# Kernel optimization log

Measured on AMD Instinct MI355X. Metric: run time of the kernel, lower is better.

The kernel has to match this reference:

```python
import jax, jax.numpy as jnp
import numpy as np

D_MODEL = 1024
NHEAD = 16
HEAD_DIM = D_MODEL // NHEAD
SCALE = HEAD_DIM ** (-0.5)


def setup_inputs() -> dict:
    key = jax.random.key(0)
    k1, k2, k3 = jax.random.split(key, 3)
    B, T, C = 2, 2048, D_MODEL
    x = jax.random.normal(k1, (B, T, C), dtype=jnp.float32)
    W_qkv = jax.random.normal(k2, (3 * C, C), dtype=jnp.float32) * (C ** -0.5)
    b_qkv = jnp.zeros((3 * C,), dtype=jnp.float32)
    W_out = jax.random.normal(k3, (C, C), dtype=jnp.float32) * (C ** -0.5)
    b_out = jnp.zeros((C,), dtype=jnp.float32)
    return {"x": x, "W_qkv": W_qkv, "b_qkv": b_qkv, "W_out": W_out, "b_out": b_out}


def reference(x, W_qkv, b_qkv, W_out, b_out):
    B, T, C = x.shape
    H, hd = NHEAD, HEAD_DIM
    qkv = x @ W_qkv.T + b_qkv
    qkv = qkv.reshape(B, T, 3, H, hd).transpose(2, 0, 3, 1, 4)
    q, k, v = qkv[0], qkv[1], qkv[2]
    # scaled dot-product scores: (B,H,T,T)
    attn = jnp.einsum('bhqd,bhkd->bhqk', q, k) * SCALE
    # causal mask (is_causal=True): lower-triangular allowed
    causal = jnp.tril(jnp.ones((T, T), dtype=bool))
    attn = jnp.where(causal[None, None, :, :], attn, -jnp.inf)
    attn = jax.nn.softmax(attn, axis=-1)
    # (B,H,T,hd) -> (B,T,C)
    out = jnp.einsum('bhqk,bhkd->bhqd', attn, v)
    out = out.transpose(0, 2, 1, 3).reshape(B, T, C)
    out = out @ W_out.T + b_out
    return out
```

## Files before the change

### kernel.cpp

```cpp
#include <hip/hip_runtime.h>
#include <hip/hip_bf16.h>
#include <stdint.h>

#define D_MODEL 1024
#define NHEAD   16
#define HEAD_DIM 64
#define BATCH   2
#define SEQ     2048
#define M_TOK   (BATCH*SEQ)
#define N_QKV   (3*D_MODEL)
#define KDIM    1024
#define Q_SCALE (0.125f * 1.44269504088896f)

typedef __bf16 bf16_t;
typedef bf16_t bf16x8 __attribute__((ext_vector_type(8)));
typedef bf16_t bf16x4 __attribute__((ext_vector_type(4)));
typedef float  f32x4  __attribute__((ext_vector_type(4)));

__device__ __forceinline__ void gl_lds16(const void* g, void* l) {
    __builtin_amdgcn_global_load_lds(
        (__attribute__((address_space(1))) void*)(void*)(const_cast<void*>(g)),
        (__attribute__((address_space(3))) void*)l, 16, 0, 0);
}

#define N4_X  (M_TOK * KDIM / 4)
#define N4_W1 (N_QKV * KDIM / 4)
#define N4_W2 (D_MODEL * KDIM / 4)
__global__ void convert_all(const float* __restrict__ x,
                            const float* __restrict__ w1,
                            const float* __restrict__ w2,
                            bf16_t* __restrict__ ox,
                            bf16_t* __restrict__ o1,
                            bf16_t* __restrict__ o2) {
    int t = blockIdx.x * blockDim.x + threadIdx.x;
    const float* src;
    bf16_t* dst;
    int off;
    if (t < N4_X)                { src = x;  dst = ox; off = t; }
    else if (t < N4_X + N4_W1)   { src = w1; dst = o1; off = t - N4_X; }
    else                         { src = w2; dst = o2; off = t - N4_X - N4_W1; }
    float4 v = reinterpret_cast<const float4*>(src)[off];
    bf16x4 o = { (bf16_t)v.x, (bf16_t)v.y, (bf16_t)v.z, (bf16_t)v.w };
    reinterpret_cast<bf16x4*>(dst)[off] = o;
}

template <int MODE>
__global__ __launch_bounds__(256) void gemm_bt(
    const bf16_t* __restrict__ A,
    const bf16_t* __restrict__ Bw,
    const float*  __restrict__ bias,
    int N,
    bf16_t* __restrict__ qkv_out,
    bf16_t* __restrict__ vt_out,
    float*  __restrict__ f32_out)
{
    __shared__ bf16_t As[128 * 32];
    __shared__ bf16_t Bs[128 * 32];

    const int cpx = gridDim.x >> 3;
    const int bid = (blockIdx.x & 7) * cpx + (blockIdx.x >> 3);

    const int nbn = N / 128;
    const int bm = bid / nbn;
    const int bn = bid % nbn;
    const int m0 = bm * 128, n0 = bn * 128;
    const int tid = threadIdx.x, wave = tid >> 6, lane = tid & 63;
    const int wr = wave >> 1, wc = wave & 1;

    f32x4 acc[4][4] = {};

    const int srow = lane >> 2;
    const int scol = ((lane & 3) ^ ((lane >> 3) & 3)) * 8;
    const bf16_t* gA0 = A  + (size_t)(m0 + wave * 16 + srow) * KDIM + scol;
    const bf16_t* gB0 = Bw + (size_t)(n0 + wave * 16 + srow) * KDIM + scol;
    bf16_t* lA0 = &As[(wave * 16) * 32];
    bf16_t* lB0 = &Bs[(wave * 16) * 32];

    const int fr = lane & 15;
    const int ch = ((lane >> 4) ^ ((fr >> 1) & 3)) * 8;

    for (int k0 = 0; k0 < KDIM; k0 += 32) {
        gl_lds16(gA0 + k0,             lA0);
        gl_lds16(gA0 + 64 * KDIM + k0, lA0 + 64 * 32);
        gl_lds16(gB0 + k0,             lB0);
        gl_lds16(gB0 + 64 * KDIM + k0, lB0 + 64 * 32);
        __syncthreads();

        bf16x8 af[4], bfr[4];
#pragma unroll
        for (int i = 0; i < 4; i++)
            af[i] = *reinterpret_cast<const bf16x8*>(
                &As[(wr * 64 + i * 16 + fr) * 32 + ch]);
#pragma unroll
        for (int j = 0; j < 4; j++)
            bfr[j] = *reinterpret_cast<const bf16x8*>(
                &Bs[(wc * 64 + j * 16 + fr) * 32 + ch]);
#pragma unroll
        for (int i = 0; i < 4; i++)
#pragma unroll
            for (int j = 0; j < 4; j++)
                acc[i][j] = __builtin_amdgcn_mfma_f32_16x16x32_bf16(
                    af[i], bfr[j], acc[i][j], 0, 0, 0);
        __syncthreads();
    }

#pragma unroll
    for (int i = 0; i < 4; i++) {
#pragma unroll
        for (int j = 0; j < 4; j++) {
            const int col = n0 + wc * 64 + j * 16 + fr;
            const float bv = bias[col];
#pragma unroll
            for (int r = 0; r < 4; r++) {
                const int row = m0 + wr * 64 + i * 16 + (lane >> 4) * 4 + r;
                float v = acc[i][j][r] + bv;
                if (MODE == 0) {
                    const int s = col >> 10;
                    if (s == 0) {
                        qkv_out[(size_t)row * N_QKV + col] = (bf16_t)(v * Q_SCALE);
                    } else if (s == 1) {
                        qkv_out[(size_t)row * N_QKV + col] = (bf16_t)v;
                    } else {
                        const int rem = col & 1023;
                        const int h = rem >> 6, d = rem & 63;
                        const int b = row >> 11, t = row & 2047;
                        vt_out[((size_t)((b * NHEAD + h) * HEAD_DIM + d)) * SEQ + t] =
                            (bf16_t)v;
                    }
                } else {
                    f32_out[(size_t)row * N + col] = v;
                }
            }
        }
    }
}

__global__ __launch_bounds__(512) void attn_fwd(
    const bf16_t* __restrict__ qkv,
    const bf16_t* __restrict__ Vt,
    bf16_t* __restrict__ O)
{
    __shared__ bf16_t Ks[2][64 * 64];
    __shared__ bf16_t Vs[2][64 * 64];
    __shared__ bf16_t Ps[8][16 * 72];

    const int nqt = SEQ / 64;
    const int nbh = BATCH * NHEAD;
    const int qt = (nqt - 1) - (blockIdx.x / nbh);
    const int bh = blockIdx.x % nbh;
    const int b = bh >> 4, h = bh & 15;
    const int q0 = qt * 64;
    const int tid = threadIdx.x, wave = tid >> 6, lane = tid & 63;
    const int group = wave >> 2;
    const int w4 = wave & 3;
    const int fr = lane & 15;
    const int kq = lane >> 4;
    const int sw = fr & 7;
    const int c0 = (kq ^ sw) * 8;
    const int c1 = ((kq + 4) ^ sw) * 8;

    bf16x8 qf[2];
    {
        const size_t qrow = (size_t)(b * SEQ + q0 + w4 * 16 + fr);
        const int cbase = h * 64 + kq * 8;
        qf[0] = *reinterpret_cast<const bf16x8*>(&qkv[qrow * N_QKV + cbase]);
        qf[1] = *reinterpret_cast<const bf16x8*>(&qkv[qrow * N_QKV + cbase + 32]);
    }

    f32x4 acc_o[4] = {};
    float l_part = 0.f;

    const int srow = lane >> 3;
    const int scol = ((lane & 7) ^ srow) * 8;
    const bf16_t* gK = qkv + (size_t)(b * SEQ) * N_QKV + (D_MODEL + h * 64);
    const bf16_t* gV = Vt + (size_t)(bh * 64) * SEQ;

    const int nh0 = (qt + 2) >> 1;
    const int my_n = (group == 0) ? nh0 : (qt + 1 - nh0);
    const int base_t = (group == 0) ? 0 : nh0;

    for (int it = 0; it < nh0; ++it) {
        const bool act = (it < my_n);
        const int g_it = base_t + it;
        const int kv0 = g_it * 64;
        if (act) {
#pragma unroll
            for (int c = 0; c < 2; c++) {
                const int row = c * 32 + w4 * 8 + srow;
                gl_lds16(gK + (size_t)(kv0 + row) * N_QKV + scol,
                         &Ks[group][(c * 32 + w4 * 8) * 64]);
                gl_lds16(gV + (size_t)row * SEQ + kv0 + scol,
                         &Vs[group][(c * 32 + w4 * 8) * 64]);
            }
        }
        __syncthreads();

        if (act) {
            f32x4 s[4];
            __builtin_amdgcn_s_setprio(1);
#pragma unroll
            for (int j = 0; j < 4; j++) {
                bf16x8 k0f = *reinterpret_cast<const bf16x8*>(
                    &Ks[group][(j * 16 + fr) * 64 + c0]);
                bf16x8 k1f = *reinterpret_cast<const bf16x8*>(
                    &Ks[group][(j * 16 + fr) * 64 + c1]);
                f32x4 t = {0.f, 0.f, 0.f, 0.f};
                t = __builtin_amdgcn_mfma_f32_16x16x32_bf16(k0f, qf[0], t, 0, 0, 0);
                t = __builtin_amdgcn_mfma_f32_16x16x32_bf16(k1f, qf[1], t, 0, 0, 0);
                s[j] = t;
            }
            __builtin_amdgcn_s_setprio(0);

            if (g_it == qt) {
                const int qg = w4 * 16 + fr;
#pragma unroll
                for (int j = 0; j < 4; j++)
#pragma unroll
                    for (int r = 0; r < 4; r++)
                        if (j * 16 + kq * 4 + r > qg) s[j][r] = -1e30f;
            }

            float rs = 0.f;
#pragma unroll
            for (int j = 0; j < 4; j++)
#pragma unroll
                for (int r = 0; r < 4; r++) {
                    const float p = exp2f(s[j][r]);
                    s[j][r] = p;
                    rs += p;
                }
            l_part += rs;

#pragma unroll
            for (int j = 0; j < 4; j++) {
                bf16x4 pq = { (bf16_t)s[j][0], (bf16_t)s[j][1],
                              (bf16_t)s[j][2], (bf16_t)s[j][3] };
                *reinterpret_cast<bf16x4*>(&Ps[wave][fr * 72 + j * 16 + kq * 4]) = pq;
            }
            bf16x8 pb0 = *reinterpret_cast<const bf16x8*>(
                &Ps[wave][fr * 72 + kq * 8]);
            bf16x8 pb1 = *reinterpret_cast<const bf16x8*>(
                &Ps[wave][fr * 72 + 32 + kq * 8]);

            __builtin_amdgcn_s_setprio(1);
#pragma unroll
            for (int j = 0; j < 4; j++) {
                bf16x8 v0f = *reinterpret_cast<const bf16x8*>(
                    &Vs[group][(j * 16 + fr) * 64 + c0]);
                bf16x8 v1f = *reinterpret_cast<const bf16x8*>(
                    &Vs[group][(j * 16 + fr) * 64 + c1]);
                acc_o[j] = __builtin_amdgcn_mfma_f32_16x16x32_bf16(v0f, pb0, acc_o[j], 0, 0, 0);
                acc_o[j] = __builtin_amdgcn_mfma_f32_16x16x32_bf16(v1f, pb1, acc_o[j], 0, 0, 0);
            }
            __builtin_amdgcn_s_setprio(0);
        }

        __syncthreads();
    }

    float* Cf = reinterpret_cast<float*>(&Ps[0][0]);
    const int pbase = w4 * 1088;
    if (group == 1) {
#pragma unroll
        for (int j = 0; j < 4; j++)
#pragma unroll
            for (int r = 0; r < 4; r++)
                Cf[pbase + (j * 4 + r) * 64 + lane] = acc_o[j][r];
        Cf[pbase + 1024 + lane] = l_part;
    }
    __syncthreads();
    if (group == 0) {
#pragma unroll
        for (int j = 0; j < 4; j++)
#pragma unroll
            for (int r = 0; r < 4; r++)
                acc_o[j][r] += Cf[pbase + (j * 4 + r) * 64 + lane];
        l_part += Cf[pbase + 1024 + lane];

        l_part += __shfl_xor(l_part, 16);
        l_part += __shfl_xor(l_part, 32);
        const float inv = 1.0f / l_part;
        const size_t rowq = (size_t)(b * SEQ + q0 + w4 * 16 + fr);
#pragma unroll
        for (int j = 0; j < 4; j++) {
            bf16x4 ov = { (bf16_t)(acc_o[j][0] * inv), (bf16_t)(acc_o[j][1] * inv),
                          (bf16_t)(acc_o[j][2] * inv), (bf16_t)(acc_o[j][3] * inv) };
            *reinterpret_cast<bf16x4*>(&O[rowq * D_MODEL + h * 64 + j * 16 + kq * 4]) = ov;
        }
    }
}

extern "C" void kernel_launch(void* const* d_in, const int* in_sizes, int n_in,
                              void* d_out, int out_size, void* d_ws, size_t ws_size,
                              hipStream_t stream) {
    (void)in_sizes; (void)n_in; (void)out_size; (void)ws_size;
    const float* x    = (const float*)d_in[0];
    const float* Wqkv = (const float*)d_in[1];
    const float* bqkv = (const float*)d_in[2];
    const float* Wout = (const float*)d_in[3];
    const float* bout = (const float*)d_in[4];
    float* out = (float*)d_out;

    char* ws = (char*)d_ws;
    size_t off = 0;
    bf16_t* x_bf    = (bf16_t*)(ws + off); off += (size_t)M_TOK * KDIM * 2;
    bf16_t* wqkv_bf = (bf16_t*)(ws + off); off += (size_t)N_QKV * KDIM * 2;
    bf16_t* wout_bf = (bf16_t*)(ws + off); off += (size_t)D_MODEL * KDIM * 2;
    bf16_t* qkv     = (bf16_t*)(ws + off); off += (size_t)M_TOK * N_QKV * 2;
    bf16_t* vt      = (bf16_t*)(ws + off); off += (size_t)BATCH * NHEAD * HEAD_DIM * SEQ * 2;
    bf16_t* o_bf    = (bf16_t*)(ws + off); off += (size_t)M_TOK * D_MODEL * 2;

    convert_all<<<(N4_X + N4_W1 + N4_W2) / 256, 256, 0, stream>>>(
        x, Wqkv, Wout, x_bf, wqkv_bf, wout_bf);

    gemm_bt<0><<<(M_TOK / 128) * (N_QKV / 128), 256, 0, stream>>>(
        x_bf, wqkv_bf, bqkv, N_QKV, qkv, vt, nullptr);

    attn_fwd<<<BATCH * NHEAD * (SEQ / 64), 512, 0, stream>>>(qkv, vt, o_bf);

    gemm_bt<1><<<(M_TOK / 128) * (D_MODEL / 128), 256, 0, stream>>>(
        o_bf, wout_bf, bout, D_MODEL, nullptr, nullptr, out);
}
```

Measured before the change: 113.9 us.

## Double GEMM K-tile to 64 with XOR swizzle, setprio, and vectorized V^T store

Raises the GEMM K-step from 32 to 64, so each barrier pair covers twice as many MFMAs and the loop runs half as many iterations. The LDS layout changes to 64-element rows with an 8-way XOR swizzle. It also raises wave priority around the MFMA block and writes the transposed V output as packed 4-element bf16 vectors instead of scalar stores. The cost is double the LDS per block and more fragment registers, which may reduce occupancy.

```diff
diff --git a/kernel.cpp b/kernel.cpp
--- a/kernel.cpp
+++ b/kernel.cpp
@@ -54,8 +54,8 @@
     bf16_t* __restrict__ vt_out,
     float*  __restrict__ f32_out)
 {
-    __shared__ bf16_t As[128 * 32];
-    __shared__ bf16_t Bs[128 * 32];
+    __shared__ bf16_t As[128 * 64];
+    __shared__ bf16_t Bs[128 * 64];
 
     const int cpx = gridDim.x >> 3;
     const int bid = (blockIdx.x & 7) * cpx + (blockIdx.x >> 3);
@@ -69,38 +69,48 @@
 
     f32x4 acc[4][4] = {};
 
-    const int srow = lane >> 2;
-    const int scol = ((lane & 3) ^ ((lane >> 3) & 3)) * 8;
-    const bf16_t* gA0 = A  + (size_t)(m0 + wave * 16 + srow) * KDIM + scol;
-    const bf16_t* gB0 = Bw + (size_t)(n0 + wave * 16 + srow) * KDIM + scol;
-    bf16_t* lA0 = &As[(wave * 16) * 32];
-    bf16_t* lB0 = &Bs[(wave * 16) * 32];
+    const int srow = lane >> 3;
+    const int scol = ((lane & 7) ^ srow) * 8;
+    const bf16_t* gA0 = A  + (size_t)(m0 + wave * 32 + srow) * KDIM + scol;
+    const bf16_t* gB0 = Bw + (size_t)(n0 + wave * 32 + srow) * KDIM + scol;
+    bf16_t* lA0 = &As[(wave * 32) * 64];
+    bf16_t* lB0 = &Bs[(wave * 32) * 64];
 
     const int fr = lane & 15;
-    const int ch = ((lane >> 4) ^ ((fr >> 1) & 3)) * 8;
-
-    for (int k0 = 0; k0 < KDIM; k0 += 32) {
-        gl_lds16(gA0 + k0,             lA0);
-        gl_lds16(gA0 + 64 * KDIM + k0, lA0 + 64 * 32);
-        gl_lds16(gB0 + k0,             lB0);
-        gl_lds16(gB0 + 64 * KDIM + k0, lB0 + 64 * 32);
+    const int kq = lane >> 4;
+
+    for (int k0 = 0; k0 < KDIM; k0 += 64) {
+#pragma unroll
+        for (int c = 0; c < 4; c++) {
+            gl_lds16(gA0 + (size_t)(c * 8) * KDIM + k0, lA0 + (c * 8) * 64);
+            gl_lds16(gB0 + (size_t)(c * 8) * KDIM + k0, lB0 + (c * 8) * 64);
+        }
         __syncthreads();
 
-        bf16x8 af[4], bfr[4];
+        bf16x8 af[2][4], bfr[2][4];
+#pragma unroll
+        for (int kk = 0; kk < 2; kk++) {
+            const int ch = (((kk << 2) | kq) ^ (fr & 7)) * 8;
+#pragma unroll
+            for (int i = 0; i < 4; i++)
+                af[kk][i] = *reinterpret_cast<const bf16x8*>(
+                    &As[(wr * 64 + i * 16 + fr) * 64 + ch]);
+#pragma unroll
+            for (int j = 0; j < 4; j++)
+                bfr[kk][j] = *reinterpret_cast<const bf16x8*>(
+                    &Bs[(wc * 64 + j * 16 + fr) * 64 + ch]);
+        }
+        __builtin_amdgcn_s_setprio(1);
 #pragma unroll
         for (int i = 0; i < 4; i++)
-            af[i] = *reinterpret_cast<const bf16x8*>(
-                &As[(wr * 64 + i * 16 + fr) * 32 + ch]);
-#pragma unroll
-        for (int j = 0; j < 4; j++)
-            bfr[j] = *reinterpret_cast<const bf16x8*>(
-                &Bs[(wc * 64 + j * 16 + fr) * 32 + ch]);
-#pragma unroll
-        for (int i = 0; i < 4; i++)
-#pragma unroll
-            for (int j = 0; j < 4; j++)
+#pragma unroll
+            for (int j = 0; j < 4; j++) {
                 acc[i][j] = __builtin_amdgcn_mfma_f32_16x16x32_bf16(
-                    af[i], bfr[j], acc[i][j], 0, 0, 0);
+                    af[0][i], bfr[0][j], acc[i][j], 0, 0, 0);
+                acc[i][j] = __builtin_amdgcn_mfma_f32_16x16x32_bf16(
+                    af[1][i], bfr[1][j], acc[i][j], 0, 0, 0);
+            }
+        __builtin_amdgcn_s_setprio(0);
         __syncthreads();
     }
 
@@ -110,26 +120,30 @@
         for (int j = 0; j < 4; j++) {
             const int col = n0 + wc * 64 + j * 16 + fr;
             const float bv = bias[col];
-#pragma unroll
-            for (int r = 0; r < 4; r++) {
-                const int row = m0 + wr * 64 + i * 16 + (lane >> 4) * 4 + r;
-                float v = acc[i][j][r] + bv;
-                if (MODE == 0) {
-                    const int s = col >> 10;
-                    if (s == 0) {
-                        qkv_out[(size_t)row * N_QKV + col] = (bf16_t)(v * Q_SCALE);
-                    } else if (s == 1) {
-                        qkv_out[(size_t)row * N_QKV + col] = (bf16_t)v;
-                    } else {
-                        const int rem = col & 1023;
-                        const int h = rem >> 6, d = rem & 63;
-                        const int b = row >> 11, t = row & 2047;
-                        vt_out[((size_t)((b * NHEAD + h) * HEAD_DIM + d)) * SEQ + t] =
-                            (bf16_t)v;
-                    }
-                } else {
-                    f32_out[(size_t)row * N + col] = v;
-                }
+            const int row0 = m0 + wr * 64 + i * 16 + kq * 4;
+            if (MODE == 1) {
+#pragma unroll
+                for (int r = 0; r < 4; r++)
+                    f32_out[(size_t)(row0 + r) * N + col] = acc[i][j][r] + bv;
+            } else if (col < 1024) {
+#pragma unroll
+                for (int r = 0; r < 4; r++)
+                    qkv_out[(size_t)(row0 + r) * N_QKV + col] =
+                        (bf16_t)((acc[i][j][r] + bv) * Q_SCALE);
+            } else if (col < 2048) {
+#pragma unroll
+                for (int r = 0; r < 4; r++)
+                    qkv_out[(size_t)(row0 + r) * N_QKV + col] =
+                        (bf16_t)(acc[i][j][r] + bv);
+            } else {
+                const int d = col & 63, hh = (col >> 6) & 15;
+                const int bb = row0 >> 11, t0 = row0 & 2047;
+                bf16x4 pv = { (bf16_t)(acc[i][j][0] + bv),
+                              (bf16_t)(acc[i][j][1] + bv),
+                              (bf16_t)(acc[i][j][2] + bv),
+                              (bf16_t)(acc[i][j][3] + bv) };
+                *reinterpret_cast<bf16x4*>(
+                    &vt_out[((size_t)((bb * NHEAD + hh) * HEAD_DIM + d)) * SEQ + t0]) = pv;
             }
         }
     }
```

New measurement: 104.9 us. 1.09x faster.
